# Kernel tuning notes

Hardware: AMD Instinct MI355X
Metric: run time of the kernel (lower is better)

Reference implementation:

```python
import jax, jax.numpy as jnp
import numpy as np

N_NODES = 100000
N_EDGES = 1600000
D_FEAT = 128
UNITS = 128
LEAKY_ALPHA = 0.2  # tf.nn.leaky_relu default


def setup_inputs() -> dict:
    key = jax.random.key(0)
    k1, k2, k3, k4 = jax.random.split(key, 4)
    node_states = jax.random.normal(k1, (N_NODES, D_FEAT), dtype=jnp.float32)
    edges = jax.random.randint(k2, (N_EDGES, 2), 0, N_NODES, dtype=jnp.int64)
    kernel = jax.random.normal(k3, (D_FEAT, UNITS), dtype=jnp.float32) * (1.0 / np.sqrt(D_FEAT))
    kernel_attention = jax.random.normal(k4, (2 * UNITS, 1), dtype=jnp.float32) * (1.0 / np.sqrt(2 * UNITS))
    return {
        "node_states": node_states,
        "edges": edges,
        "kernel": kernel,
        "kernel_attention": kernel_attention,
    }


def reference(node_states, edges, kernel, kernel_attention):
    n = node_states.shape[0]
    tgt_idx = edges[:, 0]
    src_idx = edges[:, 1]

    # node_states_transformed: [N, units]
    h = node_states @ kernel

    # Attention logits. concat([tgt, src]) @ ka == tgt @ ka_t + src @ ka_s
    # (avoids materializing the [E, 2*units] concat).
    ka_t = kernel_attention[:UNITS, 0]   # [units]
    ka_s = kernel_attention[UNITS:, 0]   # [units]
    score_t = h @ ka_t                   # [N]
    score_s = h @ ka_s                   # [N]
    e = score_t[tgt_idx] + score_s[src_idx]              # [E]
    e = jax.nn.leaky_relu(e, negative_slope=LEAKY_ALPHA)
    e = jnp.exp(jnp.clip(e, -2.0, 2.0))

    # Segment softmax over incoming edges of each target node.
    sum_e = jax.ops.segment_sum(e, tgt_idx, num_segments=n)  # [N]
    attention = e / (sum_e[tgt_idx] + 1e-9)                  # [E]

    # Weighted scatter-sum of source messages.
    messages = h[src_idx] * attention[:, None]               # [E, units]
    output = jax.ops.segment_sum(messages, tgt_idx, num_segments=n)  # [N, units]
    return output
```

## Files before the change

### kernel.cpp

```cpp
#include <hip/hip_runtime.h>
#include <stdint.h>

typedef unsigned short ushort_t;
typedef __attribute__((ext_vector_type(8))) short short8;
typedef __attribute__((ext_vector_type(4))) float float4v;

#define N_NODES 100000
#define N_EDGES 1600000
#define D 128
#define NB_GEMM 1563
#define NB_B1   250
#define EPB     6400
#define BUCKETS 782

static __device__ __forceinline__ float bf2f(uint32_t u) {
    return __builtin_bit_cast(float, u << 16);
}
static __device__ __forceinline__ ushort_t f2bf(float f) {
    uint32_t u = __builtin_bit_cast(uint32_t, f);
    uint32_t r = u + 0x7fffu + ((u >> 16) & 1u);
    return (ushort_t)(r >> 16);
}
static __device__ __forceinline__ float edge_e(float s) {
    float x = (s >= 0.0f) ? s : 0.2f * s;
    x = fminf(fmaxf(x, -2.0f), 2.0f);
    return __expf(x);
}

__global__ void __launch_bounds__(256) prep_kernel(const float* __restrict__ W,
                                                   const float* __restrict__ KA,
                                                   float* __restrict__ wa,
                                                   ushort_t* __restrict__ WT,
                                                   const int* __restrict__ E,
                                                   int* __restrict__ eflag) {
    __shared__ int s;
    int b = blockIdx.x, t = threadIdx.x;
    int i = b * 256 + t;
    if (b < 64) {
        int k = i >> 7, nn = i & 127;
        int kb = k >> 5, q = (k >> 3) & 3, j = k & 7;
        int tt = nn >> 4, l = nn & 15;
        WT[((kb * 8 + tt) * 64 + q * 16 + l) * 8 + j] = f2bf(W[i]);
    } else if (b == 64) {
        if (t == 0) s = 0;
        __syncthreads();
        int nz = 0;
#pragma unroll
        for (int j = 0; j < 8; j++)
            if (E[(t + j * 256) * 2 + 1] != 0) nz = 1;
        if (nz) atomicOr(&s, 1);
        __syncthreads();
        if (t == 0) *eflag = (s == 0) ? 1 : 0;
    } else if (b == 65) {
        int half = t >> 7, k = t & 127;
        const float* kav = KA + half * 128;
        const float* wrow = W + k * 128;
        float acc = 0.0f;
#pragma unroll 8
        for (int j = 0; j < 128; j++) acc += wrow[j] * kav[j];
        wa[half * 128 + k] = acc;
    }
}

__global__ void __launch_bounds__(256) mega1_kernel(const float* __restrict__ X,
                                                    const ushort_t* __restrict__ WT,
                                                    const float* __restrict__ wa,
                                                    ushort_t* __restrict__ H,
                                                    float* __restrict__ st,
                                                    float* __restrict__ ss,
                                                    int M,
                                                    const int* __restrict__ E,
                                                    const int* __restrict__ eflag,
                                                    int* __restrict__ sortedE,
                                                    int* __restrict__ bmatR,
                                                    int* __restrict__ lofsm) {
    __shared__ ushort_t ob[4][16 * 136];
    if (blockIdx.x >= NB_GEMM) {
        int eb = blockIdx.x - NB_GEMM;
        int t = threadIdx.x;
        int* lhist = (int*)ob;
        int* lpart = ((int*)ob) + 1024;
        for (int j = t; j < 1024; j += 256) lhist[j] = 0;
        __syncthreads();
        int i64 = *eflag;
        int base = eb * EPB;
        for (int j = 0; j < 25; j++) {
            int i = base + j * 256 + t;
            int tgt = i64 ? E[i * 4] : E[i * 2];
            if ((unsigned)tgt >= (unsigned)N_NODES) tgt = 0;
            atomicAdd(&lhist[tgt >> 7], 1);
        }
        __syncthreads();
        int c0 = lhist[t * 4], c1 = lhist[t * 4 + 1];
        int c2 = lhist[t * 4 + 2], c3 = lhist[t * 4 + 3];
        int sum = c0 + c1 + c2 + c3;
        lpart[t] = sum;
        __syncthreads();
        for (int off = 1; off < 256; off <<= 1) {
            int x = (t >= off) ? lpart[t - off] : 0;
            __syncthreads();
            lpart[t] += x;
            __syncthreads();
        }
        int e0 = lpart[t] - sum;
        int e1 = e0 + c0, e2 = e1 + c1, e3 = e2 + c2;
        int cc[4] = {c0, c1, c2, c3};
        int ee[4] = {e0, e1, e2, e3};
#pragma unroll
        for (int k = 0; k < 4; k++) {
            int bb = t * 4 + k;
            if (bb < BUCKETS) {
                bmatR[eb * BUCKETS + bb] = cc[k];
                lofsm[eb * BUCKETS + bb] = ee[k];
            }
        }
        lhist[t * 4] = e0; lhist[t * 4 + 1] = e1;
        lhist[t * 4 + 2] = e2; lhist[t * 4 + 3] = e3;
        __syncthreads();
        for (int j = 0; j < 25; j++) {
            int i = base + j * 256 + t;
            int tgt, src;
            if (i64) { tgt = E[i * 4]; src = E[i * 4 + 2]; }
            else     { tgt = E[i * 2]; src = E[i * 2 + 1]; }
            if ((unsigned)tgt >= (unsigned)N_NODES) tgt = 0;
            if ((unsigned)src >= (unsigned)N_NODES) src = 0;
            int pos = atomicAdd(&lhist[tgt >> 7], 1);
            if (pos < EPB) sortedE[base + pos] = ((tgt & 127) << 17) | src;
        }
        return;
    }
    int tid = threadIdx.x;
    int wave = tid >> 6, lane = tid & 63;
    int quad = lane >> 4, l16 = lane & 15;
    int m0 = blockIdx.x * 64 + wave * 16;

    int arow = m0 + l16; if (arow >= M) arow = M - 1;
    const float* xrow = X + (size_t)arow * D + quad * 8;
    short8 a[4];
    float sct = 0.0f, scs = 0.0f;
#pragma unroll
    for (int kb = 0; kb < 4; kb++) {
        float4 f0 = *(const float4*)(xrow + kb * 32);
        float4 f1 = *(const float4*)(xrow + kb * 32 + 4);
        const float* wt0 = wa + kb * 32 + quad * 8;
        float4 t0 = *(const float4*)(wt0);
        float4 t1 = *(const float4*)(wt0 + 4);
        float4 s0 = *(const float4*)(wt0 + 128);
        float4 s1 = *(const float4*)(wt0 + 132);
        sct += f0.x * t0.x + f0.y * t0.y + f0.z * t0.z + f0.w * t0.w
             + f1.x * t1.x + f1.y * t1.y + f1.z * t1.z + f1.w * t1.w;
        scs += f0.x * s0.x + f0.y * s0.y + f0.z * s0.z + f0.w * s0.w
             + f1.x * s1.x + f1.y * s1.y + f1.z * s1.z + f1.w * s1.w;
        short8 v;
        v[0] = (short)f2bf(f0.x); v[1] = (short)f2bf(f0.y);
        v[2] = (short)f2bf(f0.z); v[3] = (short)f2bf(f0.w);
        v[4] = (short)f2bf(f1.x); v[5] = (short)f2bf(f1.y);
        v[6] = (short)f2bf(f1.z); v[7] = (short)f2bf(f1.w);
        a[kb] = v;
    }
    sct += __shfl_xor(sct, 16); sct += __shfl_xor(sct, 32);
    scs += __shfl_xor(scs, 16); scs += __shfl_xor(scs, 32);
    if (quad == 0 && m0 + l16 < M) { st[m0 + l16] = sct; ss[m0 + l16] = scs; }

    const short8* Bf = (const short8*)WT;
    float4v acc[8] = {};
#pragma unroll
    for (int kb = 0; kb < 4; kb++) {
#pragma unroll
        for (int t = 0; t < 8; t++) {
            short8 b = Bf[(kb * 8 + t) * 64 + lane];
            acc[t] = __builtin_amdgcn_mfma_f32_16x16x32_bf16(a[kb], b, acc[t], 0, 0, 0);
        }
    }
    ushort_t* obw = ob[wave];
#pragma unroll
    for (int t = 0; t < 8; t++)
#pragma unroll
        for (int r = 0; r < 4; r++)
            obw[(quad * 4 + r) * 136 + t * 16 + l16] = f2bf(acc[t][r]);
    __syncthreads();
#pragma unroll
    for (int p = 0; p < 4; p++) {
        int row = p * 4 + quad;
        int orow = m0 + row;
        if (orow < M) {
            uint4 v = *(const uint4*)(&obw[row * 136 + l16 * 8]);
            *(uint4*)(H + (size_t)orow * D + l16 * 8) = v;
        }
    }
}

__global__ void __launch_bounds__(256) scanb_kernel(const int* __restrict__ bmatR,
                                                    int* __restrict__ offm,
                                                    int* __restrict__ bt) {
    __shared__ int l[256];
    int b = blockIdx.x, t = threadIdx.x;
    int v = (t < NB_B1) ? bmatR[t * BUCKETS + b] : 0;
    l[t] = v;
    __syncthreads();
    for (int off = 1; off < 256; off <<= 1) {
        int x = (t >= off) ? l[t - off] : 0;
        __syncthreads();
        l[t] += x;
        __syncthreads();
    }
    offm[b * 256 + t] = l[t] - v;
    if (t == 255) bt[b] = l[255];
}

__global__ void __launch_bounds__(1024) scan2_kernel(const int* __restrict__ bt,
                                                     int* __restrict__ bbase,
                                                     int* __restrict__ rowp) {
    __shared__ int l[1024];
    int t = threadIdx.x;
    int v = (t < BUCKETS) ? bt[t] : 0;
    l[t] = v;
    __syncthreads();
    for (int off = 1; off < 1024; off <<= 1) {
        int x = (t >= off) ? l[t - off] : 0;
        __syncthreads();
        l[t] += x;
        __syncthreads();
    }
    if (t < BUCKETS) bbase[t] = l[t] - v;
    if (t == BUCKETS - 1) bbase[BUCKETS] = l[t];
    if (t == 0) rowp[N_NODES] = N_EDGES;
}

__global__ void __launch_bounds__(256) csrb_kernel(const int* __restrict__ sortedE,
                                                   const int* __restrict__ bmatR,
                                                   const int* __restrict__ lofsm,
                                                   const int* __restrict__ offm,
                                                   const int* __restrict__ bbase,
                                                   int* __restrict__ rowp,
                                                   int* __restrict__ csr_src) {
    __shared__ int stage[4096];
    __shared__ int lh[128];
    __shared__ int lsc[128];
    int b = blockIdx.x, t = threadIdx.x;
    int gbase = bbase[b];
    int total = bbase[b + 1] - gbase;
    if (total > 4096) total = 4096;
    int soff = offm[b * 256 + t];
    int slen = 0, sstart = 0;
    if (t < NB_B1) {
        sstart = lofsm[t * BUCKETS + b];
        slen   = bmatR[t * BUCKETS + b];
    }
    for (int k = 0; k < slen; k++) {
        int idx = soff + k;
        if (idx < 4096) stage[idx] = sortedE[t * EPB + sstart + k];
    }
    if (t < 128) lh[t] = 0;
    __syncthreads();
    for (int j = t; j < total; j += 256) atomicAdd(&lh[stage[j] >> 17], 1);
    __syncthreads();
    int v = (t < 128) ? lh[t] : 0;
    if (t < 128) lsc[t] = v;
    __syncthreads();
    for (int off = 1; off < 128; off <<= 1) {
        int x = (t >= off && t < 128) ? lsc[t - off] : 0;
        __syncthreads();
        if (t < 128) lsc[t] += x;
        __syncthreads();
    }
    if (t < 128) {
        int node = b * 128 + t;
        int ex = lsc[t] - v;
        if (node < N_NODES) rowp[node] = gbase + ex;
        lh[t] = ex;
    }
    __syncthreads();
    for (int j = t; j < total; j += 256) {
        int p = stage[j];
        int pos = atomicAdd(&lh[p >> 17], 1);
        if (pos < total) csr_src[gbase + pos] = p & 0x1FFFF;
    }
}

__global__ void __launch_bounds__(256) agg_kernel(const int* __restrict__ rowp,
                                                  const int* __restrict__ csr_src,
                                                  const float* __restrict__ st,
                                                  const float* __restrict__ ss,
                                                  const ushort_t* __restrict__ H,
                                                  float* __restrict__ out, int n) {
    int wave = threadIdx.x >> 6, lane = threadIdx.x & 63;
    int node = blockIdx.x * 4 + wave;
    if (node >= n) return;
    node = __builtin_amdgcn_readfirstlane(node);
    int g = lane >> 4, l = lane & 15;
    int start = rowp[node];
    int end   = rowp[node + 1];
    float stn = st[node];
    float den = 0.0f;
    float acc[8] = {};
    for (int m = start + g; m < end; m += 4) {
        int src = csr_src[m];
        float e = edge_e(stn + ss[src]);
        den += e;
        uint4 p = *(const uint4*)(H + (size_t)src * D + l * 8);
        acc[0] += e * bf2f(p.x & 0xffff); acc[1] += e * bf2f(p.x >> 16);
        acc[2] += e * bf2f(p.y & 0xffff); acc[3] += e * bf2f(p.y >> 16);
        acc[4] += e * bf2f(p.z & 0xffff); acc[5] += e * bf2f(p.z >> 16);
        acc[6] += e * bf2f(p.w & 0xffff); acc[7] += e * bf2f(p.w >> 16);
    }
    den += __shfl_xor(den, 16);
    den += __shfl_xor(den, 32);
#pragma unroll
    for (int j = 0; j < 8; j++) {
        acc[j] += __shfl_xor(acc[j], 16);
        acc[j] += __shfl_xor(acc[j], 32);
    }
    float inv = 1.0f / (den + 1e-9f);
    if (g == 0) {
        float4 o0 = make_float4(acc[0] * inv, acc[1] * inv, acc[2] * inv, acc[3] * inv);
        float4 o1 = make_float4(acc[4] * inv, acc[5] * inv, acc[6] * inv, acc[7] * inv);
        *(float4*)(out + (size_t)node * D + l * 8) = o0;
        *(float4*)(out + (size_t)node * D + l * 8 + 4) = o1;
    }
}

extern "C" void kernel_launch(void* const* d_in, const int* in_sizes, int n_in,
                              void* d_out, int out_size, void* d_ws, size_t ws_size,
                              hipStream_t stream) {
    const float* X  = (const float*)d_in[0];
    const int*   E  = (const int*)d_in[1];
    const float* W  = (const float*)d_in[2];
    const float* KA = (const float*)d_in[3];
    for (int i = 0; i < n_in; i++) {
        int s = in_sizes[i];
        if (s == N_NODES * D)      X  = (const float*)d_in[i];
        else if (s == N_EDGES * 2) E  = (const int*)d_in[i];
        else if (s == D * D)       W  = (const float*)d_in[i];
        else if (s == 2 * D)       KA = (const float*)d_in[i];
    }
    float* out = (float*)d_out;
    char* ob = (char*)d_out;
    int* sortedE = (int*)(ob + 0);
    int* bmatR   = (int*)(ob + 6400000);
    int* lofsm   = (int*)(ob + 7200768);
    int* offm    = (int*)(ob + 8001536);
    int* bt      = (int*)(ob + 8802304);
    int* bbase   = (int*)(ob + 8805432);

    char* ws = (char*)d_ws;
    ushort_t* H        = (ushort_t*)(ws + 0);
    float*    wa       = (float*)   (ws + 25600000);
    float*    st       = (float*)   (ws + 25601024);
    float*    ssb      = (float*)   (ws + 26001024);
    int*      rowp     = (int*)     (ws + 26801024);
    int*      csrs     = (int*)     (ws + 27201040);
    int*      eflag    = (int*)     (ws + 33601040);
    ushort_t* WT       = (ushort_t*)(ws + 33602656);

    const int NB_WAVE = (N_NODES + 3) / 4;

    prep_kernel<<<66, 256, 0, stream>>>(W, KA, wa, WT, E, eflag);
    mega1_kernel<<<NB_GEMM + NB_B1, 256, 0, stream>>>(X, WT, wa, H, st, ssb,
                                                      N_NODES, E, eflag,
                                                      sortedE, bmatR, lofsm);
    scanb_kernel<<<BUCKETS, 256, 0, stream>>>(bmatR, offm, bt);
    scan2_kernel<<<1, 1024, 0, stream>>>(bt, bbase, rowp);
    csrb_kernel<<<BUCKETS, 256, 0, stream>>>(sortedE, bmatR, lofsm, offm,
                                             bbase, rowp, csrs);
    agg_kernel<<<NB_WAVE, 256, 0, stream>>>(rowp, csrs, st, ssb, H, out, N_NODES);
}
```

Measured before the change: 241.0 us.

## Process two GEMM tiles per block with prefetch and unroll aggregation by two

The projection part of the fused kernel now launches about half as many GEMM blocks. Each block handles two 64-row tiles and prefetches the second tile's X rows while the first is computed. The __syncthreads before the H store is dropped, which is safe because each wave uses only its own LDS slice. The aggregation loop handles two edges per iteration, using packed float2 FMAs and 32-bit index math, to expose more independent memory loads and cut ALU work.

```diff
diff --git a/kernel.cpp b/kernel.cpp
--- a/kernel.cpp
+++ b/kernel.cpp
@@ -4,17 +4,25 @@
 typedef unsigned short ushort_t;
 typedef __attribute__((ext_vector_type(8))) short short8;
 typedef __attribute__((ext_vector_type(4))) float float4v;
+typedef __attribute__((ext_vector_type(2))) float float2v;
 
 #define N_NODES 100000
 #define N_EDGES 1600000
 #define D 128
 #define NB_GEMM 1563
+#define NBP     782
 #define NB_B1   250
 #define EPB     6400
 #define BUCKETS 782
 
 static __device__ __forceinline__ float bf2f(uint32_t u) {
     return __builtin_bit_cast(float, u << 16);
+}
+static __device__ __forceinline__ float2v up2(uint32_t u) {
+    float2v r;
+    r.x = __builtin_bit_cast(float, u << 16);
+    r.y = __builtin_bit_cast(float, u & 0xffff0000u);
+    return r;
 }
 static __device__ __forceinline__ ushort_t f2bf(float f) {
     uint32_t u = __builtin_bit_cast(uint32_t, f);
@@ -75,8 +83,8 @@
                                                     int* __restrict__ bmatR,
                                                     int* __restrict__ lofsm) {
     __shared__ ushort_t ob[4][16 * 136];
-    if (blockIdx.x >= NB_GEMM) {
-        int eb = blockIdx.x - NB_GEMM;
+    if (blockIdx.x >= NBP) {
+        int eb = blockIdx.x - NBP;
         int t = threadIdx.x;
         int* lhist = (int*)ob;
         int* lpart = ((int*)ob) + 1024;
@@ -132,60 +140,85 @@
     int tid = threadIdx.x;
     int wave = tid >> 6, lane = tid & 63;
     int quad = lane >> 4, l16 = lane & 15;
-    int m0 = blockIdx.x * 64 + wave * 16;
-
-    int arow = m0 + l16; if (arow >= M) arow = M - 1;
-    const float* xrow = X + (size_t)arow * D + quad * 8;
-    short8 a[4];
-    float sct = 0.0f, scs = 0.0f;
-#pragma unroll
-    for (int kb = 0; kb < 4; kb++) {
-        float4 f0 = *(const float4*)(xrow + kb * 32);
-        float4 f1 = *(const float4*)(xrow + kb * 32 + 4);
-        const float* wt0 = wa + kb * 32 + quad * 8;
-        float4 t0 = *(const float4*)(wt0);
-        float4 t1 = *(const float4*)(wt0 + 4);
-        float4 s0 = *(const float4*)(wt0 + 128);
-        float4 s1 = *(const float4*)(wt0 + 132);
-        sct += f0.x * t0.x + f0.y * t0.y + f0.z * t0.z + f0.w * t0.w
-             + f1.x * t1.x + f1.y * t1.y + f1.z * t1.z + f1.w * t1.w;
-        scs += f0.x * s0.x + f0.y * s0.y + f0.z * s0.z + f0.w * s0.w
-             + f1.x * s1.x + f1.y * s1.y + f1.z * s1.z + f1.w * s1.w;
-        short8 v;
-        v[0] = (short)f2bf(f0.x); v[1] = (short)f2bf(f0.y);
-        v[2] = (short)f2bf(f0.z); v[3] = (short)f2bf(f0.w);
-        v[4] = (short)f2bf(f1.x); v[5] = (short)f2bf(f1.y);
-        v[6] = (short)f2bf(f1.z); v[7] = (short)f2bf(f1.w);
-        a[kb] = v;
-    }
-    sct += __shfl_xor(sct, 16); sct += __shfl_xor(sct, 32);
-    scs += __shfl_xor(scs, 16); scs += __shfl_xor(scs, 32);
-    if (quad == 0 && m0 + l16 < M) { st[m0 + l16] = sct; ss[m0 + l16] = scs; }
-
+    ushort_t* obw = ob[wave];
     const short8* Bf = (const short8*)WT;
-    float4v acc[8] = {};
-#pragma unroll
-    for (int kb = 0; kb < 4; kb++) {
-#pragma unroll
-        for (int t = 0; t < 8; t++) {
-            short8 b = Bf[(kb * 8 + t) * 64 + lane];
-            acc[t] = __builtin_amdgcn_mfma_f32_16x16x32_bf16(a[kb], b, acc[t], 0, 0, 0);
-        }
-    }
-    ushort_t* obw = ob[wave];
-#pragma unroll
-    for (int t = 0; t < 8; t++)
-#pragma unroll
-        for (int r = 0; r < 4; r++)
-            obw[(quad * 4 + r) * 136 + t * 16 + l16] = f2bf(acc[t][r]);
-    __syncthreads();
-#pragma unroll
-    for (int p = 0; p < 4; p++) {
-        int row = p * 4 + quad;
-        int orow = m0 + row;
-        if (orow < M) {
-            uint4 v = *(const uint4*)(&obw[row * 136 + l16 * 8]);
-            *(uint4*)(H + (size_t)orow * D + l16 * 8) = v;
+
+    int t0 = blockIdx.x;
+    int nt = (t0 + NBP < NB_GEMM) ? 2 : 1;
+
+    float4 f[8];
+    {
+        int ar = t0 * 64 + wave * 16 + l16; if (ar >= M) ar = M - 1;
+        const float* xr = X + (size_t)ar * D + quad * 8;
+#pragma unroll
+        for (int kb = 0; kb < 4; kb++) {
+            f[kb * 2]     = *(const float4*)(xr + kb * 32);
+            f[kb * 2 + 1] = *(const float4*)(xr + kb * 32 + 4);
+        }
+    }
+    for (int it = 0; it < nt; it++) {
+        int m0 = (t0 + it * NBP) * 64 + wave * 16;
+        float4 nf[8];
+        if (it + 1 < nt) {
+            int ar = (t0 + NBP) * 64 + wave * 16 + l16; if (ar >= M) ar = M - 1;
+            const float* xr = X + (size_t)ar * D + quad * 8;
+#pragma unroll
+            for (int kb = 0; kb < 4; kb++) {
+                nf[kb * 2]     = *(const float4*)(xr + kb * 32);
+                nf[kb * 2 + 1] = *(const float4*)(xr + kb * 32 + 4);
+            }
+        }
+        short8 a[4];
+        float sct = 0.0f, scs = 0.0f;
+#pragma unroll
+        for (int kb = 0; kb < 4; kb++) {
+            float4 f0 = f[kb * 2], f1 = f[kb * 2 + 1];
+            const float* wt0 = wa + kb * 32 + quad * 8;
+            float4 t0v = *(const float4*)(wt0);
+            float4 t1v = *(const float4*)(wt0 + 4);
+            float4 s0v = *(const float4*)(wt0 + 128);
+            float4 s1v = *(const float4*)(wt0 + 132);
+            sct += f0.x * t0v.x + f0.y * t0v.y + f0.z * t0v.z + f0.w * t0v.w
+                 + f1.x * t1v.x + f1.y * t1v.y + f1.z * t1v.z + f1.w * t1v.w;
+            scs += f0.x * s0v.x + f0.y * s0v.y + f0.z * s0v.z + f0.w * s0v.w
+                 + f1.x * s1v.x + f1.y * s1v.y + f1.z * s1v.z + f1.w * s1v.w;
+            short8 v;
+            v[0] = (short)f2bf(f0.x); v[1] = (short)f2bf(f0.y);
+            v[2] = (short)f2bf(f0.z); v[3] = (short)f2bf(f0.w);
+            v[4] = (short)f2bf(f1.x); v[5] = (short)f2bf(f1.y);
+            v[6] = (short)f2bf(f1.z); v[7] = (short)f2bf(f1.w);
+            a[kb] = v;
+        }
+        sct += __shfl_xor(sct, 16); sct += __shfl_xor(sct, 32);
+        scs += __shfl_xor(scs, 16); scs += __shfl_xor(scs, 32);
+        if (quad == 0 && m0 + l16 < M) { st[m0 + l16] = sct; ss[m0 + l16] = scs; }
+
+        float4v acc[8] = {};
+#pragma unroll
+        for (int kb = 0; kb < 4; kb++) {
+#pragma unroll
+            for (int t = 0; t < 8; t++) {
+                short8 b = Bf[(kb * 8 + t) * 64 + lane];
+                acc[t] = __builtin_amdgcn_mfma_f32_16x16x32_bf16(a[kb], b, acc[t], 0, 0, 0);
+            }
+        }
+#pragma unroll
+        for (int t = 0; t < 8; t++)
+#pragma unroll
+            for (int r = 0; r < 4; r++)
+                obw[(quad * 4 + r) * 136 + t * 16 + l16] = f2bf(acc[t][r]);
+#pragma unroll
+        for (int p = 0; p < 4; p++) {
+            int row = p * 4 + quad;
+            int orow = m0 + row;
+            if (orow < M) {
+                uint4 v = *(const uint4*)(&obw[row * 136 + l16 * 8]);
+                *(uint4*)(H + (size_t)orow * D + l16 * 8) = v;
+            }
+        }
+        if (it + 1 < nt) {
+#pragma unroll
+            for (int j = 0; j < 8; j++) f[j] = nf[j];
         }
     }
 }
@@ -293,28 +326,46 @@
     int end   = rowp[node + 1];
     float stn = st[node];
     float den = 0.0f;
-    float acc[8] = {};
-    for (int m = start + g; m < end; m += 4) {
-        int src = csr_src[m];
-        float e = edge_e(stn + ss[src]);
-        den += e;
-        uint4 p = *(const uint4*)(H + (size_t)src * D + l * 8);
-        acc[0] += e * bf2f(p.x & 0xffff); acc[1] += e * bf2f(p.x >> 16);
-        acc[2] += e * bf2f(p.y & 0xffff); acc[3] += e * bf2f(p.y >> 16);
-        acc[4] += e * bf2f(p.z & 0xffff); acc[5] += e * bf2f(p.z >> 16);
-        acc[6] += e * bf2f(p.w & 0xffff); acc[7] += e * bf2f(p.w >> 16);
+    float2v acc2[4] = {};
+    int m = start + g;
+    for (; m + 4 < end; m += 8) {
+        int s0 = csr_src[m], s1 = csr_src[m + 4];
+        float e0 = edge_e(stn + ss[s0]);
+        float e1 = edge_e(stn + ss[s1]);
+        den += e0 + e1;
+        uint4 p0 = *(const uint4*)(H + ((unsigned)s0 << 7) + l * 8);
+        uint4 p1 = *(const uint4*)(H + ((unsigned)s1 << 7) + l * 8);
+        float2v E0 = {e0, e0}, E1 = {e1, e1};
+        acc2[0] += E0 * up2(p0.x) + E1 * up2(p1.x);
+        acc2[1] += E0 * up2(p0.y) + E1 * up2(p1.y);
+        acc2[2] += E0 * up2(p0.z) + E1 * up2(p1.z);
+        acc2[3] += E0 * up2(p0.w) + E1 * up2(p1.w);
+    }
+    if (m < end) {
+        int s0 = csr_src[m];
+        float e0 = edge_e(stn + ss[s0]);
+        den += e0;
+        uint4 p0 = *(const uint4*)(H + ((unsigned)s0 << 7) + l * 8);
+        float2v E0 = {e0, e0};
+        acc2[0] += E0 * up2(p0.x);
+        acc2[1] += E0 * up2(p0.y);
+        acc2[2] += E0 * up2(p0.z);
+        acc2[3] += E0 * up2(p0.w);
     }
     den += __shfl_xor(den, 16);
     den += __shfl_xor(den, 32);
-#pragma unroll
-    for (int j = 0; j < 8; j++) {
-        acc[j] += __shfl_xor(acc[j], 16);
-        acc[j] += __shfl_xor(acc[j], 32);
+    float r[8];
+#pragma unroll
+    for (int j = 0; j < 4; j++) {
+        float a0 = acc2[j].x, a1 = acc2[j].y;
+        a0 += __shfl_xor(a0, 16); a0 += __shfl_xor(a0, 32);
+        a1 += __shfl_xor(a1, 16); a1 += __shfl_xor(a1, 32);
+        r[j * 2] = a0; r[j * 2 + 1] = a1;
     }
     float inv = 1.0f / (den + 1e-9f);
     if (g == 0) {
-        float4 o0 = make_float4(acc[0] * inv, acc[1] * inv, acc[2] * inv, acc[3] * inv);
-        float4 o1 = make_float4(acc[4] * inv, acc[5] * inv, acc[6] * inv, acc[7] * inv);
+        float4 o0 = make_float4(r[0] * inv, r[1] * inv, r[2] * inv, r[3] * inv);
+        float4 o1 = make_float4(r[4] * inv, r[5] * inv, r[6] * inv, r[7] * inv);
         *(float4*)(out + (size_t)node * D + l * 8) = o0;
         *(float4*)(out + (size_t)node * D + l * 8 + 4) = o1;
     }
@@ -356,9 +407,9 @@
     const int NB_WAVE = (N_NODES + 3) / 4;
 
     prep_kernel<<<66, 256, 0, stream>>>(W, KA, wa, WT, E, eflag);
-    mega1_kernel<<<NB_GEMM + NB_B1, 256, 0, stream>>>(X, WT, wa, H, st, ssb,
-                                                      N_NODES, E, eflag,
-                                                      sortedE, bmatR, lofsm);
+    mega1_kernel<<<NBP + NB_B1, 256, 0, stream>>>(X, WT, wa, H, st, ssb,
+                                                  N_NODES, E, eflag,
+                                                  sortedE, bmatR, lofsm);
     scanb_kernel<<<BUCKETS, 256, 0, stream>>>(bmatR, offm, bt);
     scan2_kernel<<<1, 1024, 0, stream>>>(bt, bbase, rowp);
     csrb_kernel<<<BUCKETS, 256, 0, stream>>>(sortedE, bmatR, lofsm, offm,
```

After: 235.7 us. 2.2% less time.
